# Kernel tuning notes

Hardware: AMD Instinct MI355X
Metric: run time of the kernel (lower is better)

Reference implementation:

```python
import jax, jax.numpy as jnp
import numpy as np
import math

D_MODEL = 1024
NUM_HEADS = 16
D_K = D_MODEL // NUM_HEADS
MAX_LEN = 2048
B, S = 2, 1024


def setup_inputs() -> dict:
    key = jax.random.key(0)
    ks = jax.random.split(key, 10)
    lin_scale = 1.0 / math.sqrt(D_MODEL)
    # torch Linear: weight (out, in), y = x @ W.T + b
    Wq = jax.random.uniform(ks[0], (D_MODEL, D_MODEL), jnp.float32, -lin_scale, lin_scale)
    Wk = jax.random.uniform(ks[1], (D_MODEL, D_MODEL), jnp.float32, -lin_scale, lin_scale)
    Wv = jax.random.uniform(ks[2], (D_MODEL, D_MODEL), jnp.float32, -lin_scale, lin_scale)
    Wo = jax.random.uniform(ks[3], (D_MODEL, D_MODEL), jnp.float32, -lin_scale, lin_scale)
    bq = jnp.zeros((D_MODEL,), jnp.float32)
    bk = jnp.zeros((D_MODEL,), jnp.float32)
    bv = jnp.zeros((D_MODEL,), jnp.float32)
    bo = jnp.zeros((D_MODEL,), jnp.float32)
    # xavier_uniform for Er (max_len, d_k)
    er_bound = math.sqrt(6.0 / (MAX_LEN + D_K))
    Er = jax.random.uniform(ks[4], (MAX_LEN, D_K), jnp.float32, -er_bound, er_bound)
    x = jax.random.normal(ks[5], (B, S, D_MODEL), jnp.float32)
    return {"x": x, "Wq": Wq, "bq": bq, "Wk": Wk, "bk": bk,
            "Wv": Wv, "bv": bv, "Wo": Wo, "bo": bo, "Er": Er}


def reference(x, Wq, bq, Wk, bk, Wv, bv, Wo, bo, Er):
    Bsz, Slen, Dm = x.shape
    H, dk = NUM_HEADS, D_K

    def proj(W, b):
        y = jnp.einsum('bsd,ed->bse', x, W) + b
        return y.reshape(Bsz, Slen, H, dk).transpose(0, 2, 1, 3)  # (B,H,S,dk)

    Q = proj(Wq, bq)
    K = proj(Wk, bk)
    V = proj(Wv, bv)

    # content-content scores
    AC = jnp.einsum('bhid,bhjd->bhij', Q, K)  # (B,H,S,S)

    # relative position embeddings for distances S-1 .. -(S-1)
    rel_pos = jnp.arange(Slen - 1, -Slen, -1)  # (2S-1,)
    idx = rel_pos + (Slen - 1)                 # map to 0..2S-2 (requires 2S-1 <= max_len)
    Er_emb = Er[idx]                           # (2S-1, dk)
    BD_full = jnp.einsum('bhid,md->bhim', Q, Er_emb)  # (B,H,S,2S-1)

    # relative shift: final[i,j] = BD_full[i, S-1 - i + j] (column for distance i-j)
    i_idx = jnp.arange(Slen)[:, None]                  # (S,1)
    m_idx = (Slen - 1) - i_idx + jnp.arange(Slen)[None, :]  # (S,S)
    BD = BD_full[:, :, i_idx, m_idx]                   # (B,H,S,S)

    scores = (AC + BD) / math.sqrt(dk)
    attn = jax.nn.softmax(scores, axis=-1)  # dropout is identity at eval
    out = jnp.einsum('bhij,bhjd->bhid', attn, V)       # (B,H,S,dk)
    out = out.transpose(0, 2, 1, 3).reshape(Bsz, Slen, Dm)
    return jnp.einsum('bsd,ed->bse', out, Wo) + bo
```

## Files before the change

kernel.cpp:

```cpp
#include <hip/hip_runtime.h>
#include <hip/hip_bf16.h>
#include <math.h>

#define D_MODEL 1024
#define NUM_HEADS 16
#define D_K 64
#define SEQ 1024
#define BATCH 2

typedef __hip_bfloat16 bf16;
typedef __bf16 bf16x8 __attribute__((ext_vector_type(8)));
typedef __bf16 bf16x4 __attribute__((ext_vector_type(4)));
typedef float floatx4 __attribute__((ext_vector_type(4)));

__device__ __forceinline__ floatx4 mfma16(bf16x8 a, bf16x8 b, floatx4 c) {
    return __builtin_amdgcn_mfma_f32_16x16x32_bf16(a, b, c, 0, 0, 0);
}

__global__ void detect_dtype_kernel(const void* __restrict__ x, int* __restrict__ flag) {
    __shared__ int cnt[256];
    const float* xf = (const float*)x;
    const int tid = threadIdx.x;
    int sane = 0;
    for (int i = tid; i < 4096; i += 256) {
        float v = xf[i];
        float a = fabsf(v);
        if (v == 0.0f || (a > 1e-8f && a < 1e8f)) sane++;
    }
    cnt[tid] = sane;
    __syncthreads();
    for (int s = 128; s > 0; s >>= 1) {
        if (tid < s) cnt[tid] += cnt[tid + s];
        __syncthreads();
    }
    if (tid == 0) flag[0] = (cnt[0] > 3686) ? 1 : 0;
}

struct ConvSrcs { const void* p[10]; };

__global__ __launch_bounds__(256) void convert_all_kernel(ConvSrcs srcs,
                                                          bf16* __restrict__ dstbase,
                                                          const int* __restrict__ flag) {
    const long long e = ((long long)blockIdx.x * 256 + threadIdx.x) * 8;
    int seg; long long base;
    if      (e < 2097152LL) { seg = 0; base = 0; }
    else if (e < 3145728LL) { seg = 1; base = 2097152LL; }
    else if (e < 4194304LL) { seg = 2; base = 3145728LL; }
    else if (e < 5242880LL) { seg = 3; base = 4194304LL; }
    else if (e < 6291456LL) { seg = 4; base = 5242880LL; }
    else if (e < 6292480LL) { seg = 5; base = 6291456LL; }
    else if (e < 6293504LL) { seg = 6; base = 6292480LL; }
    else if (e < 6294528LL) { seg = 7; base = 6293504LL; }
    else if (e < 6295552LL) { seg = 8; base = 6294528LL; }
    else                    { seg = 9; base = 6295552LL; }
    const long long local = e - base;
    __bf16 tmp[8];
    if (*flag) {
        const float* s = (const float*)srcs.p[seg] + local;
#pragma unroll
        for (int t = 0; t < 8; ++t) tmp[t] = (__bf16)s[t];
        *(bf16x8*)(void*)(dstbase + e) = *(const bf16x8*)tmp;
    } else {
        *(bf16x8*)(void*)(dstbase + e) =
            *(const bf16x8*)(const void*)((const bf16*)srcs.p[seg] + local);
    }
}

__global__ __launch_bounds__(256) void gemm_qkv_kernel(const bf16* __restrict__ x,
        const bf16* __restrict__ Wq, const bf16* __restrict__ Wk, const bf16* __restrict__ Wv,
        const bf16* __restrict__ bq, const bf16* __restrict__ bk, const bf16* __restrict__ bv,
        bf16* __restrict__ Qb, bf16* __restrict__ Kb, bf16* __restrict__ Vt) {
    const int wsel = blockIdx.x >> 4;
    const int n0 = (blockIdx.x & 15) * 64;
    const int m0 = blockIdx.y * 128;
    const bf16* W    = (wsel == 0) ? Wq : ((wsel == 1) ? Wk : Wv);
    const bf16* bias = (wsel == 0) ? bq : ((wsel == 1) ? bk : bv);

    __shared__ __bf16 As[128][72];
    __shared__ __bf16 Bs[64][72];
    const int tid = threadIdx.x;
    const int wave = tid >> 6, lane = tid & 63, quad = lane >> 4, l16 = lane & 15;
    const int wr = (wave >> 1) * 64, wc = (wave & 1) * 32;
    const int arow = tid >> 1, acg = (tid & 1) * 32;
    const int brow = tid >> 2, bcg = (tid & 3) * 16;

    floatx4 acc[4][2];
#pragma unroll
    for (int r = 0; r < 4; ++r)
#pragma unroll
        for (int c = 0; c < 2; ++c) acc[r][c] = (floatx4)0.f;

    for (int k0 = 0; k0 < 1024; k0 += 64) {
        const bf16* ag = x + (size_t)(m0 + arow) * 1024 + k0 + acg;
        const bf16* bg = W + (size_t)(n0 + brow) * 1024 + k0 + bcg;
        bf16x8 av[4], bv2[2];
#pragma unroll
        for (int c = 0; c < 4; ++c) av[c] = *(const bf16x8*)(const void*)(ag + c * 8);
#pragma unroll
        for (int c = 0; c < 2; ++c) bv2[c] = *(const bf16x8*)(const void*)(bg + c * 8);
        __syncthreads();
#pragma unroll
        for (int c = 0; c < 4; ++c) *(bf16x8*)&As[arow][acg + c * 8] = av[c];
#pragma unroll
        for (int c = 0; c < 2; ++c) *(bf16x8*)&Bs[brow][bcg + c * 8] = bv2[c];
        __syncthreads();
#pragma unroll
        for (int kk = 0; kk < 2; ++kk) {
            bf16x8 af[4], bfr[2];
#pragma unroll
            for (int r = 0; r < 4; ++r)
                af[r] = *(const bf16x8*)&As[wr + r * 16 + l16][kk * 32 + quad * 8];
#pragma unroll
            for (int c = 0; c < 2; ++c)
                bfr[c] = *(const bf16x8*)&Bs[wc + c * 16 + l16][kk * 32 + quad * 8];
#pragma unroll
            for (int r = 0; r < 4; ++r)
#pragma unroll
                for (int c = 0; c < 2; ++c)
                    acc[r][c] = mfma16(af[r], bfr[c], acc[r][c]);
        }
    }

    if (wsel < 2) {
        bf16* Cb = (wsel == 0) ? Qb : Kb;
#pragma unroll
        for (int c = 0; c < 2; ++c) {
            const int col = n0 + wc + c * 16 + l16;
            const float bvl = (float)bias[col];
#pragma unroll
            for (int r = 0; r < 4; ++r)
#pragma unroll
                for (int v = 0; v < 4; ++v) {
                    const int row = m0 + wr + r * 16 + quad * 4 + v;
                    Cb[(size_t)row * 1024 + col] = (bf16)(acc[r][c][v] + bvl);
                }
        }
    } else {
        __bf16* Ls = &As[0][0];
        __syncthreads();
#pragma unroll
        for (int c = 0; c < 2; ++c) {
            const int col = wc + c * 16 + l16;
            const float bvl = (float)bias[n0 + col];
#pragma unroll
            for (int r = 0; r < 4; ++r)
#pragma unroll
                for (int v = 0; v < 4; ++v) {
                    const int row = wr + r * 16 + quad * 4 + v;
                    Ls[col * 132 + row] = (__bf16)(acc[r][c][v] + bvl);
                }
        }
        __syncthreads();
        const int b = m0 >> 10, s0 = m0 & 1023, h = n0 >> 6;
        const int d = tid >> 2, sg = (tid & 3) * 32;
        bf16* g = Vt + ((size_t)((b * NUM_HEADS + h) * 64 + d)) * SEQ + s0 + sg;
#pragma unroll
        for (int c = 0; c < 32; c += 8)
            *(bf16x8*)(void*)(g + c) = *(const bf16x8*)&Ls[d * 132 + sg + c];
    }
}

__global__ __launch_bounds__(256, 3) void attn_mfma_kernel(const bf16* __restrict__ Q,
                                                           const bf16* __restrict__ Kc,
                                                           const bf16* __restrict__ Vt,
                                                           const bf16* __restrict__ Er,
                                                           bf16* __restrict__ Opart,
                                                           float* __restrict__ Ml) {
    const int i0 = blockIdx.x * 128;
    const int h = blockIdx.y;
    const int zz = blockIdx.z;
    const int b = zz / 3, jsel = zz - b * 3;
    const int tid = threadIdx.x;
    const int wave = tid >> 6, lane = tid & 63, quad = lane >> 4, l16 = lane & 15;

    const int jbeg = (jsel == 0) ? 0 : ((jsel == 1) ? 384 : 704);
    const int nt   = (jsel == 0) ? 6 : 5;

    __shared__ __bf16 Ks[64][72];
    __shared__ __bf16 Vs[80][72];
    __shared__ __bf16 scr_all[4][3264];
    __bf16* scr = &scr_all[wave][0];
    __bf16* Qs = &scr_all[0][0];

    for (int e = tid; e < 16 * 72; e += 256) {
        const int r = e / 72, c = e - r * 72;
        Vs[64 + r][c] = (r == 0) ? (__bf16)1.0f : (__bf16)0.0f;
    }
    {
        const int r = tid >> 1, cg = (tid & 1) * 32;
        const bf16* g = Q + ((size_t)(b * SEQ + i0 + r)) * D_MODEL + h * 64 + cg;
#pragma unroll
        for (int c = 0; c < 32; c += 8)
            *(bf16x8*)(void*)(Qs + r * 72 + cg + c) = *(const bf16x8*)(const void*)(g + c);
    }
    __syncthreads();
    bf16x8 aq[2][2];
#pragma unroll
    for (int half = 0; half < 2; ++half)
#pragma unroll
        for (int kk = 0; kk < 2; ++kk)
            aq[half][kk] = *(const bf16x8*)(const void*)(
                Qs + (wave * 32 + half * 16 + l16) * 72 + kk * 32 + quad * 8);

    floatx4 oacc[5][2];
#pragma unroll
    for (int ct = 0; ct < 5; ++ct)
#pragma unroll
        for (int half = 0; half < 2; ++half) oacc[ct][half] = (floatx4)0.f;

    const int eb = 960 + i0;
    const bf16* Kg = Kc + (size_t)b * SEQ * D_MODEL + h * 64;
    const bf16* Vtg = Vt + (size_t)((b * NUM_HEADS + h) * 64) * SEQ;

    const int r4 = tid >> 2, c4 = (tid & 3) * 16;
    bf16x8 kp0, kp1, vp0, vp1;
    {
        const bf16* kg = Kg + (size_t)(jbeg + r4) * D_MODEL + c4;
        const bf16* vg = Vtg + (size_t)r4 * SEQ + jbeg + c4;
        kp0 = *(const bf16x8*)(const void*)kg;
        kp1 = *(const bf16x8*)(const void*)(kg + 8);
        vp0 = *(const bf16x8*)(const void*)vg;
        vp1 = *(const bf16x8*)(const void*)(vg + 8);
    }

    for (int t = 0; t < nt; ++t) {
        const int j0 = jbeg + t * 64;
        __syncthreads();
        *(bf16x8*)&Ks[r4][c4]     = kp0;
        *(bf16x8*)&Ks[r4][c4 + 8] = kp1;
        *(bf16x8*)&Vs[r4][c4]     = vp0;
        *(bf16x8*)&Vs[r4][c4 + 8] = vp1;
        __syncthreads();
        if (t < nt - 1) {
            const int jn = j0 + 64;
            const bf16* kg = Kg + (size_t)(jn + r4) * D_MODEL + c4;
            const bf16* vg = Vtg + (size_t)r4 * SEQ + jn + c4;
            kp0 = *(const bf16x8*)(const void*)kg;
            kp1 = *(const bf16x8*)(const void*)(kg + 8);
            vp0 = *(const bf16x8*)(const void*)vg;
            vp1 = *(const bf16x8*)(const void*)(vg + 8);
        }

#pragma unroll
        for (int ct = 0; ct < 6; ++ct) {
            const int erow = eb - j0 + wave * 32 + ct * 16 + l16;
            const bf16* ep = Er + (size_t)erow * 64 + quad * 8;
            bf16x8 be0 = *(const bf16x8*)(const void*)ep;
            bf16x8 be1 = *(const bf16x8*)(const void*)(ep + 32);
#pragma unroll
            for (int half = 0; half < 2; ++half) {
                floatx4 tv = (floatx4)0.f;
                tv = mfma16(aq[half][0], be0, tv);
                tv = mfma16(aq[half][1], be1, tv);
                bf16x4 tb;
#pragma unroll
                for (int v = 0; v < 4; ++v) tb[v] = (__bf16)tv[v];
                *(bf16x4*)(void*)(scr + (ct * 16 + l16) * 34 + half * 16 + quad * 4) = tb;
            }
        }
        floatx4 sfrag[4][2];
#pragma unroll
        for (int ct = 0; ct < 4; ++ct) {
            bf16x8 bk0 = *(const bf16x8*)&Ks[ct * 16 + l16][quad * 8];
            bf16x8 bk1 = *(const bf16x8*)&Ks[ct * 16 + l16][32 + quad * 8];
#pragma unroll
            for (int half = 0; half < 2; ++half) {
                floatx4 s = (floatx4)0.f;
                s = mfma16(aq[half][0], bk0, s);
                s = mfma16(aq[half][1], bk1, s);
                sfrag[ct][half] = s;
            }
        }
#pragma unroll
        for (int ct = 0; ct < 4; ++ct)
#pragma unroll
            for (int half = 0; half < 2; ++half)
#pragma unroll
                for (int v = 0; v < 4; ++v) {
                    const int rl = half * 16 + quad * 4 + v;
                    const int cl = 63 + rl - (ct * 16 + l16);
                    sfrag[ct][half][v] =
                        (sfrag[ct][half][v] + (float)scr[cl * 34 + rl]) * 0.125f;
                }
#pragma unroll
        for (int ct = 0; ct < 4; ++ct)
#pragma unroll
            for (int half = 0; half < 2; ++half)
#pragma unroll
                for (int v = 0; v < 4; ++v) {
                    const int rl = half * 16 + quad * 4 + v;
                    scr[rl * 72 + ct * 16 + l16] = (__bf16)__expf(sfrag[ct][half][v]);
                }
        bf16x8 ap[2][2];
#pragma unroll
        for (int half = 0; half < 2; ++half)
#pragma unroll
            for (int kk = 0; kk < 2; ++kk)
                ap[half][kk] = *(const bf16x8*)(const void*)(
                    scr + (half * 16 + l16) * 72 + kk * 32 + quad * 8);
#pragma unroll
        for (int ct = 0; ct < 5; ++ct) {
            bf16x8 bv0 = *(const bf16x8*)&Vs[ct * 16 + l16][quad * 8];
            bf16x8 bv1 = *(const bf16x8*)&Vs[ct * 16 + l16][32 + quad * 8];
#pragma unroll
            for (int half = 0; half < 2; ++half) {
                oacc[ct][half] = mfma16(ap[half][0], bv0, oacc[ct][half]);
                oacc[ct][half] = mfma16(ap[half][1], bv1, oacc[ct][half]);
            }
        }
    }

    bf16* Op = Opart + (size_t)jsel * 2097152;
#pragma unroll
    for (int ct = 0; ct < 4; ++ct)
#pragma unroll
        for (int half = 0; half < 2; ++half)
#pragma unroll
            for (int v = 0; v < 4; ++v) {
                const int row = i0 + wave * 32 + half * 16 + quad * 4 + v;
                const int col = h * 64 + ct * 16 + l16;
                Op[((size_t)(b * SEQ + row)) * D_MODEL + col] = (bf16)oacc[ct][half][v];
            }
    if (l16 == 0) {
        const int base = ((jsel * 2 + b) * 16 + h) * 1024;
#pragma unroll
        for (int half = 0; half < 2; ++half)
#pragma unroll
            for (int v = 0; v < 4; ++v) {
                const int ig = i0 + wave * 32 + half * 16 + quad * 4 + v;
                Ml[base + ig] = oacc[4][half][v];
            }
    }
}

__global__ __launch_bounds__(256) void combine_kernel(const bf16* __restrict__ Opart,
                                                      const float* __restrict__ Ml,
                                                      bf16* __restrict__ Ob) {
    const int e = (blockIdx.x * 256 + threadIdx.x) * 4;
    const int row = e >> 10, col = e & 1023;
    const int b = row >> 10, i = row & 1023, h = col >> 6;
    float l = 0.f;
#pragma unroll
    for (int s = 0; s < 3; ++s) l += Ml[(((s * 2 + b) * 16 + h) << 10) + i];
    const float inv = 1.0f / l;
    bf16x4 o1 = *(const bf16x4*)(const void*)(Opart + e);
    bf16x4 o2 = *(const bf16x4*)(const void*)(Opart + 2097152 + e);
    bf16x4 o3 = *(const bf16x4*)(const void*)(Opart + 4194304 + e);
    bf16x4 o;
#pragma unroll
    for (int v = 0; v < 4; ++v)
        o[v] = (__bf16)(((float)o1[v] + (float)o2[v] + (float)o3[v]) * inv);
    *(bf16x4*)(void*)(Ob + e) = o;
}

__global__ __launch_bounds__(256) void gemm_out_kernel(const bf16* __restrict__ A,
        const bf16* __restrict__ W, const bf16* __restrict__ bias,
        void* __restrict__ C, const int* __restrict__ flag) {
    const int n0 = blockIdx.x * 64;
    const int m0 = blockIdx.y * 64;
    __shared__ __bf16 As[64][72];
    __shared__ __bf16 Bs[64][72];
    const int tid = threadIdx.x;
    const int wave = tid >> 6, lane = tid & 63, quad = lane >> 4, l16 = lane & 15;
    const int wr = (wave >> 1) * 32, wc = (wave & 1) * 32;
    const int srow = tid >> 2, scg = (tid & 3) * 16;

    floatx4 acc[2][2];
#pragma unroll
    for (int r = 0; r < 2; ++r)
#pragma unroll
        for (int c = 0; c < 2; ++c) acc[r][c] = (floatx4)0.f;

    for (int k0 = 0; k0 < 1024; k0 += 64) {
        const bf16* ag = A + (size_t)(m0 + srow) * 1024 + k0 + scg;
        const bf16* bg = W + (size_t)(n0 + srow) * 1024 + k0 + scg;
        bf16x8 av0 = *(const bf16x8*)(const void*)ag;
        bf16x8 av1 = *(const bf16x8*)(const void*)(ag + 8);
        bf16x8 bv0 = *(const bf16x8*)(const void*)bg;
        bf16x8 bv1 = *(const bf16x8*)(const void*)(bg + 8);
        __syncthreads();
        *(bf16x8*)&As[srow][scg]     = av0;
        *(bf16x8*)&As[srow][scg + 8] = av1;
        *(bf16x8*)&Bs[srow][scg]     = bv0;
        *(bf16x8*)&Bs[srow][scg + 8] = bv1;
        __syncthreads();
#pragma unroll
        for (int kk = 0; kk < 2; ++kk) {
            bf16x8 af[2], bfr[2];
#pragma unroll
            for (int r = 0; r < 2; ++r)
                af[r] = *(const bf16x8*)&As[wr + r * 16 + l16][kk * 32 + quad * 8];
#pragma unroll
            for (int c = 0; c < 2; ++c)
                bfr[c] = *(const bf16x8*)&Bs[wc + c * 16 + l16][kk * 32 + quad * 8];
#pragma unroll
            for (int r = 0; r < 2; ++r)
#pragma unroll
                for (int c = 0; c < 2; ++c)
                    acc[r][c] = mfma16(af[r], bfr[c], acc[r][c]);
        }
    }
#pragma unroll
    for (int c = 0; c < 2; ++c) {
        const int col = n0 + wc + c * 16 + l16;
        const float bvl = (float)bias[col];
#pragma unroll
        for (int r = 0; r < 2; ++r)
#pragma unroll
            for (int v = 0; v < 4; ++v) {
                const int row = m0 + wr + r * 16 + quad * 4 + v;
                const float val = acc[r][c][v] + bvl;
                const size_t idx = (size_t)row * 1024 + col;
                if (*flag) ((float*)C)[idx] = val;
                else       ((bf16*)C)[idx] = (bf16)val;
            }
    }
}

extern "C" void kernel_launch(void* const* d_in, const int* in_sizes, int n_in,
                              void* d_out, int out_size, void* d_ws, size_t ws_size,
                              hipStream_t stream) {
    const size_t E_X = 2097152;
    const size_t E_CANON = 6426624;

    char* ws = (char*)d_ws;
    int* flag = (int*)ws;
    bf16* canon = (bf16*)(ws + 16);
    bf16* xc  = canon;
    bf16* Wqc = canon + 2097152;
    bf16* Wkc = canon + 3145728;
    bf16* Wvc = canon + 4194304;
    bf16* Woc = canon + 5242880;
    bf16* bqc = canon + 6291456;
    bf16* bkc = canon + 6292480;
    bf16* bvc = canon + 6293504;
    bf16* boc = canon + 6294528;
    bf16* Erc = canon + 6295552;
    bf16* p = canon + E_CANON;
    bf16* Qb    = p;  p += E_X;
    bf16* Kb    = p;  p += E_X;
    bf16* Vt    = p;  p += E_X;
    bf16* Opart = p;  p += 3 * E_X;
    float* Ml   = (float*)p;

    detect_dtype_kernel<<<1, 256, 0, stream>>>(d_in[0], flag);

    ConvSrcs cs;
    cs.p[0] = d_in[0]; cs.p[1] = d_in[1]; cs.p[2] = d_in[3]; cs.p[3] = d_in[5];
    cs.p[4] = d_in[7]; cs.p[5] = d_in[2]; cs.p[6] = d_in[4]; cs.p[7] = d_in[6];
    cs.p[8] = d_in[8]; cs.p[9] = d_in[9];
    convert_all_kernel<<<3138, 256, 0, stream>>>(cs, canon, flag);

    gemm_qkv_kernel<<<dim3(48, 16), 256, 0, stream>>>(xc, Wqc, Wkc, Wvc,
                                                      bqc, bkc, bvc, Qb, Kb, Vt);

    attn_mfma_kernel<<<dim3(8, 16, 6), 256, 0, stream>>>(Qb, Kb, Vt, Erc, Opart, Ml);

    combine_kernel<<<2048, 256, 0, stream>>>(Opart, Ml, Qb);

    gemm_out_kernel<<<dim3(16, 32), 256, 0, stream>>>(Qb, Woc, boc, d_out, flag);
}
```

Measured before the change: 187.8 us.

## Read K/V fragments directly from global memory and split keys into four chunks

The attention kernel no longer stages K and V tiles through shared memory. Each wave now loads its MFMA B-fragments for K, V and Q straight from global memory, which removes the per-tile barriers and the register prefetch. The key range is split into four equal 256-key chunks instead of three uneven ones, giving more blocks at higher occupancy (launch bound 4). The row-sum ones matrix moves into a small dedicated shared buffer. The cost is duplicated global/L2 traffic across waves and a fourth partial buffer for the combine kernel to read.

```diff
diff --git a/kernel.cpp b/kernel.cpp
--- a/kernel.cpp
+++ b/kernel.cpp
@@ -160,7 +160,7 @@
     }
 }
 
-__global__ __launch_bounds__(256, 3) void attn_mfma_kernel(const bf16* __restrict__ Q,
+__global__ __launch_bounds__(256, 4) void attn_mfma_kernel(const bf16* __restrict__ Q,
                                                            const bf16* __restrict__ Kc,
                                                            const bf16* __restrict__ Vt,
                                                            const bf16* __restrict__ Er,
@@ -168,39 +168,28 @@
                                                            float* __restrict__ Ml) {
     const int i0 = blockIdx.x * 128;
     const int h = blockIdx.y;
-    const int zz = blockIdx.z;
-    const int b = zz / 3, jsel = zz - b * 3;
+    const int b = blockIdx.z >> 2, jsel = blockIdx.z & 3;
     const int tid = threadIdx.x;
     const int wave = tid >> 6, lane = tid & 63, quad = lane >> 4, l16 = lane & 15;
 
-    const int jbeg = (jsel == 0) ? 0 : ((jsel == 1) ? 384 : 704);
-    const int nt   = (jsel == 0) ? 6 : 5;
-
-    __shared__ __bf16 Ks[64][72];
-    __shared__ __bf16 Vs[80][72];
     __shared__ __bf16 scr_all[4][3264];
+    __shared__ __bf16 ones[16][72];
     __bf16* scr = &scr_all[wave][0];
-    __bf16* Qs = &scr_all[0][0];
-
-    for (int e = tid; e < 16 * 72; e += 256) {
-        const int r = e / 72, c = e - r * 72;
-        Vs[64 + r][c] = (r == 0) ? (__bf16)1.0f : (__bf16)0.0f;
-    }
-    {
-        const int r = tid >> 1, cg = (tid & 1) * 32;
-        const bf16* g = Q + ((size_t)(b * SEQ + i0 + r)) * D_MODEL + h * 64 + cg;
-#pragma unroll
-        for (int c = 0; c < 32; c += 8)
-            *(bf16x8*)(void*)(Qs + r * 72 + cg + c) = *(const bf16x8*)(const void*)(g + c);
-    }
+
+    for (int e = tid; e < 16 * 72; e += 256)
+        (&ones[0][0])[e] = (e < 72) ? (__bf16)1.0f : (__bf16)0.0f;
     __syncthreads();
+
     bf16x8 aq[2][2];
 #pragma unroll
     for (int half = 0; half < 2; ++half)
 #pragma unroll
-        for (int kk = 0; kk < 2; ++kk)
-            aq[half][kk] = *(const bf16x8*)(const void*)(
-                Qs + (wave * 32 + half * 16 + l16) * 72 + kk * 32 + quad * 8);
+        for (int kk = 0; kk < 2; ++kk) {
+            const bf16* qp = Q +
+                ((size_t)(b * SEQ + i0 + wave * 32 + half * 16 + l16)) * D_MODEL +
+                h * 64 + kk * 32 + quad * 8;
+            aq[half][kk] = *(const bf16x8*)(const void*)qp;
+        }
 
     floatx4 oacc[5][2];
 #pragma unroll
@@ -211,35 +200,10 @@
     const int eb = 960 + i0;
     const bf16* Kg = Kc + (size_t)b * SEQ * D_MODEL + h * 64;
     const bf16* Vtg = Vt + (size_t)((b * NUM_HEADS + h) * 64) * SEQ;
-
-    const int r4 = tid >> 2, c4 = (tid & 3) * 16;
-    bf16x8 kp0, kp1, vp0, vp1;
-    {
-        const bf16* kg = Kg + (size_t)(jbeg + r4) * D_MODEL + c4;
-        const bf16* vg = Vtg + (size_t)r4 * SEQ + jbeg + c4;
-        kp0 = *(const bf16x8*)(const void*)kg;
-        kp1 = *(const bf16x8*)(const void*)(kg + 8);
-        vp0 = *(const bf16x8*)(const void*)vg;
-        vp1 = *(const bf16x8*)(const void*)(vg + 8);
-    }
-
-    for (int t = 0; t < nt; ++t) {
+    const int jbeg = jsel * 256;
+
+    for (int t = 0; t < 4; ++t) {
         const int j0 = jbeg + t * 64;
-        __syncthreads();
-        *(bf16x8*)&Ks[r4][c4]     = kp0;
-        *(bf16x8*)&Ks[r4][c4 + 8] = kp1;
-        *(bf16x8*)&Vs[r4][c4]     = vp0;
-        *(bf16x8*)&Vs[r4][c4 + 8] = vp1;
-        __syncthreads();
-        if (t < nt - 1) {
-            const int jn = j0 + 64;
-            const bf16* kg = Kg + (size_t)(jn + r4) * D_MODEL + c4;
-            const bf16* vg = Vtg + (size_t)r4 * SEQ + jn + c4;
-            kp0 = *(const bf16x8*)(const void*)kg;
-            kp1 = *(const bf16x8*)(const void*)(kg + 8);
-            vp0 = *(const bf16x8*)(const void*)vg;
-            vp1 = *(const bf16x8*)(const void*)(vg + 8);
-        }
 
 #pragma unroll
         for (int ct = 0; ct < 6; ++ct) {
@@ -261,8 +225,9 @@
         floatx4 sfrag[4][2];
 #pragma unroll
         for (int ct = 0; ct < 4; ++ct) {
-            bf16x8 bk0 = *(const bf16x8*)&Ks[ct * 16 + l16][quad * 8];
-            bf16x8 bk1 = *(const bf16x8*)&Ks[ct * 16 + l16][32 + quad * 8];
+            const bf16* kp = Kg + (size_t)(j0 + ct * 16 + l16) * D_MODEL + quad * 8;
+            bf16x8 bk0 = *(const bf16x8*)(const void*)kp;
+            bf16x8 bk1 = *(const bf16x8*)(const void*)(kp + 32);
 #pragma unroll
             for (int half = 0; half < 2; ++half) {
                 floatx4 s = (floatx4)0.f;
@@ -299,13 +264,23 @@
                 ap[half][kk] = *(const bf16x8*)(const void*)(
                     scr + (half * 16 + l16) * 72 + kk * 32 + quad * 8);
 #pragma unroll
-        for (int ct = 0; ct < 5; ++ct) {
-            bf16x8 bv0 = *(const bf16x8*)&Vs[ct * 16 + l16][quad * 8];
-            bf16x8 bv1 = *(const bf16x8*)&Vs[ct * 16 + l16][32 + quad * 8];
+        for (int ct = 0; ct < 4; ++ct) {
+            const bf16* vp = Vtg + (size_t)(ct * 16 + l16) * SEQ + j0 + quad * 8;
+            bf16x8 bv0 = *(const bf16x8*)(const void*)vp;
+            bf16x8 bv1 = *(const bf16x8*)(const void*)(vp + 32);
 #pragma unroll
             for (int half = 0; half < 2; ++half) {
                 oacc[ct][half] = mfma16(ap[half][0], bv0, oacc[ct][half]);
                 oacc[ct][half] = mfma16(ap[half][1], bv1, oacc[ct][half]);
+            }
+        }
+        {
+            bf16x8 bo0 = *(const bf16x8*)&ones[l16][quad * 8];
+            bf16x8 bo1 = *(const bf16x8*)&ones[l16][32 + quad * 8];
+#pragma unroll
+            for (int half = 0; half < 2; ++half) {
+                oacc[4][half] = mfma16(ap[half][0], bo0, oacc[4][half]);
+                oacc[4][half] = mfma16(ap[half][1], bo1, oacc[4][half]);
             }
         }
     }
@@ -341,16 +316,19 @@
     const int b = row >> 10, i = row & 1023, h = col >> 6;
     float l = 0.f;
 #pragma unroll
-    for (int s = 0; s < 3; ++s) l += Ml[(((s * 2 + b) * 16 + h) << 10) + i];
+    for (int s = 0; s < 4; ++s) l += Ml[(((s * 2 + b) * 16 + h) << 10) + i];
     const float inv = 1.0f / l;
-    bf16x4 o1 = *(const bf16x4*)(const void*)(Opart + e);
-    bf16x4 o2 = *(const bf16x4*)(const void*)(Opart + 2097152 + e);
-    bf16x4 o3 = *(const bf16x4*)(const void*)(Opart + 4194304 + e);
-    bf16x4 o;
-#pragma unroll
-    for (int v = 0; v < 4; ++v)
-        o[v] = (__bf16)(((float)o1[v] + (float)o2[v] + (float)o3[v]) * inv);
-    *(bf16x4*)(void*)(Ob + e) = o;
+    float o[4] = {0.f, 0.f, 0.f, 0.f};
+#pragma unroll
+    for (int s = 0; s < 4; ++s) {
+        bf16x4 ov = *(const bf16x4*)(const void*)(Opart + (size_t)s * 2097152 + e);
+#pragma unroll
+        for (int v = 0; v < 4; ++v) o[v] += (float)ov[v];
+    }
+    bf16x4 r;
+#pragma unroll
+    for (int v = 0; v < 4; ++v) r[v] = (__bf16)(o[v] * inv);
+    *(bf16x4*)(void*)(Ob + e) = r;
 }
 
 __global__ __launch_bounds__(256) void gemm_out_kernel(const bf16* __restrict__ A,
@@ -440,7 +418,7 @@
     bf16* Qb    = p;  p += E_X;
     bf16* Kb    = p;  p += E_X;
     bf16* Vt    = p;  p += E_X;
-    bf16* Opart = p;  p += 3 * E_X;
+    bf16* Opart = p;  p += 4 * E_X;
     float* Ml   = (float*)p;
 
     detect_dtype_kernel<<<1, 256, 0, stream>>>(d_in[0], flag);
@@ -454,7 +432,7 @@
     gemm_qkv_kernel<<<dim3(48, 16), 256, 0, stream>>>(xc, Wqc, Wkc, Wvc,
                                                       bqc, bkc, bvc, Qb, Kb, Vt);
 
-    attn_mfma_kernel<<<dim3(8, 16, 6), 256, 0, stream>>>(Qb, Kb, Vt, Erc, Opart, Ml);
+    attn_mfma_kernel<<<dim3(8, 16, 8), 256, 0, stream>>>(Qb, Kb, Vt, Erc, Opart, Ml);
 
     combine_kernel<<<2048, 256, 0, stream>>>(Opart, Ml, Qb);
 
```

Result: slower. 227.3 us (+21.1%).
